# Optimization experiments

Hardware: AMD Instinct MI355X
Metric: run time of the kernel (lower is better)

The kernel has to match this reference:

```python
import jax, jax.numpy as jnp
import numpy as np

B, N, E, D = 1, 50000, 800000, 128


def _mlp(x, w1, b1, w2, b2, w3, b3):
    # MLP(in, hidden, out, l=2): Linear+ReLU, Linear+ReLU, Linear
    h = jax.nn.relu(x @ w1 + b1)
    h = jax.nn.relu(h @ w2 + b2)
    return h @ w3 + b3


def _glorot(key, shape):
    fan_in, fan_out = shape[0], shape[1]
    lim = np.sqrt(6.0 / (fan_in + fan_out)).astype(np.float32)
    return jax.random.uniform(key, shape, jnp.float32, -lim, lim)


def setup_inputs() -> dict:
    key = jax.random.key(0)
    ks = jax.random.split(key, 16)
    inp = {
        "nodes": jax.random.normal(ks[0], (B, N, D), jnp.float32),
        "senders": jax.random.randint(ks[1], (E,), 0, N, jnp.int32),
        "receivers": jax.random.randint(ks[2], (E,), 0, N, jnp.int32),
        # message MLP params: 2D -> D -> D -> D
        "mw1": _glorot(ks[3], (2 * D, D)), "mb1": jnp.zeros((D,), jnp.float32),
        "mw2": _glorot(ks[4], (D, D)),     "mb2": jnp.zeros((D,), jnp.float32),
        "mw3": _glorot(ks[5], (D, D)),     "mb3": jnp.zeros((D,), jnp.float32),
        # node MLP params: 2D -> D -> D -> D
        "nw1": _glorot(ks[6], (2 * D, D)), "nb1": jnp.zeros((D,), jnp.float32),
        "nw2": _glorot(ks[7], (D, D)),     "nb2": jnp.zeros((D,), jnp.float32),
        "nw3": _glorot(ks[8], (D, D)),     "nb3": jnp.zeros((D,), jnp.float32),
    }
    return inp


def reference(nodes, senders, receivers,
              mw1, mb1, mw2, mb2, mw3, mb3,
              nw1, nb1, nw2, nb2, nw3, nb3):
    # gather endpoint features: [B, E, 2D]
    edge_in = jnp.concatenate((nodes[:, receivers], nodes[:, senders]), axis=-1)
    messages = _mlp(edge_in, mw1, mb1, mw2, mb2, mw3, mb3)  # [B, E, D]
    # scatter-add messages into receiver inbox: [B, N, D]
    inbox = jnp.zeros_like(nodes).at[:, receivers].add(messages)
    node_in = jnp.concatenate((nodes, inbox), axis=-1)  # [B, N, 2D]
    return nodes + _mlp(node_in, nw1, nb1, nw2, nb2, nw3, nb3)
```

## Files before the change

### kernel.cpp

```cpp
#include <hip/hip_runtime.h>
#include <hip/hip_bf16.h>
#include <stdint.h>

typedef __bf16 bf16;
typedef bf16 bf16x8 __attribute__((ext_vector_type(8)));
typedef float f32x4 __attribute__((ext_vector_type(4)));

#define N_NODES 50000
#define FEAT 128
#define NB_SCAN ((N_NODES + 1023) / 1024)

static constexpr size_t UV_BYTES    = (size_t)N_NODES * 256 * 2;
static constexpr size_t INBOX_BYTES = (size_t)N_NODES * FEAT * 4;

#define WUV_OFF 0
#define WM2_OFF 32768
#define WM3_OFF 49152
#define WN1_OFF 65536
#define WN2_OFF 98304
#define WN3_OFF 114688
#define W_TOTAL 131072
static constexpr size_t W_BYTES = (size_t)W_TOTAL * 2;
#define PREP_BLOCKS ((W_TOTAL + 255) / 256)

__device__ __forceinline__ bf16x8 cvt_f32x8_bf16(const float* __restrict__ p) {
  float4 f0 = *(const float4*)p;
  float4 f1 = *(const float4*)(p + 4);
  bf16x8 t;
  t[0] = (bf16)f0.x; t[1] = (bf16)f0.y; t[2] = (bf16)f0.z; t[3] = (bf16)f0.w;
  t[4] = (bf16)f1.x; t[5] = (bf16)f1.y; t[6] = (bf16)f1.z; t[7] = (bf16)f1.w;
  return t;
}

__global__ void prep_hist_kernel(const float* __restrict__ mw1, const float* __restrict__ mw2,
                                 const float* __restrict__ mw3, const float* __restrict__ nw1,
                                 const float* __restrict__ nw2, const float* __restrict__ nw3,
                                 bf16* __restrict__ w,
                                 const int* __restrict__ receivers, int* __restrict__ cnt, int E) {
  const int b = blockIdx.x;
  if (b < PREP_BLOCKS) {
    int i = b * 256 + threadIdx.x;
    if (i >= W_TOTAL) return;
    float v;
    if (i < WM2_OFF) {
      int c = i >> 7, k = i & 127;
      v = (c < 128) ? mw1[k * 128 + c] : mw1[(128 + k) * 128 + (c - 128)];
    } else if (i < WM3_OFF) {
      int j = i - WM2_OFF; int c = j >> 7, k = j & 127;
      v = mw2[k * 128 + c];
    } else if (i < WN1_OFF) {
      int j = i - WM3_OFF; int c = j >> 7, k = j & 127;
      v = mw3[k * 128 + c];
    } else if (i < WN2_OFF) {
      int j = i - WN1_OFF; int c = j >> 8, k = j & 255;
      v = nw1[k * 128 + c];
    } else if (i < WN3_OFF) {
      int j = i - WN2_OFF; int c = j >> 7, k = j & 127;
      v = nw2[k * 128 + c];
    } else {
      int j = i - WN3_OFF; int c = j >> 7, k = j & 127;
      v = nw3[k * 128 + c];
    }
    w[i] = (bf16)v;
  } else {
    int i = (b - PREP_BLOCKS) * 256 + threadIdx.x;
    if (i < E) atomicAdd(&cnt[receivers[i]], 1);
  }
}

__global__ __launch_bounds__(1024) void scan1_kernel(const int* __restrict__ cnt,
                                                     int* __restrict__ offs,
                                                     int* __restrict__ bsum) {
  __shared__ int s[1024];
  const int tid = threadIdx.x;
  const int g = blockIdx.x * 1024 + tid;
  int x = (g < N_NODES) ? cnt[g] : 0;
  s[tid] = x;
  __syncthreads();
  for (int off = 1; off < 1024; off <<= 1) {
    int v = (tid >= off) ? s[tid - off] : 0;
    __syncthreads();
    s[tid] += v;
    __syncthreads();
  }
  if (g < N_NODES) offs[g] = s[tid] - x;
  if (tid == 1023) bsum[blockIdx.x] = s[tid];
}

__global__ void scan2_kernel(int* __restrict__ bsum) {
  __shared__ int s[64];
  const int tid = threadIdx.x;
  int x = (tid < NB_SCAN) ? bsum[tid] : 0;
  s[tid] = x;
  __syncthreads();
  for (int off = 1; off < 64; off <<= 1) {
    int v = (tid >= off) ? s[tid - off] : 0;
    __syncthreads();
    s[tid] += v;
    __syncthreads();
  }
  if (tid < NB_SCAN) bsum[tid] = s[tid] - x;
}

__global__ void scatter_inbox_kernel(const int* __restrict__ senders,
                                     const int* __restrict__ receivers,
                                     const int* __restrict__ offs, const int* __restrict__ bsum,
                                     int* __restrict__ cur,
                                     int* __restrict__ sSend, int* __restrict__ sRecv,
                                     const int* __restrict__ cnt, const float* __restrict__ mb3,
                                     float* __restrict__ inbox, int E) {
  const int SC = (E + 255) >> 8;
  const int b = blockIdx.x;
  if (b < SC) {
    int i = b * 256 + threadIdx.x;
    if (i < E) {
      int r = receivers[i];
      int slot = offs[r] + bsum[r >> 10] + atomicAdd(&cur[r], 1);
      sSend[slot] = senders[i];
      sRecv[slot] = r;
    }
  } else {
    int i = (b - SC) * 256 + threadIdx.x;
    if (i >= N_NODES * 32) return;
    int n = i >> 5, q = i & 31;
    float c = (float)cnt[n];
    float4 bb = *(const float4*)(mb3 + q * 4);
    float4 o = {c * bb.x, c * bb.y, c * bb.z, c * bb.w};
    *(float4*)(inbox + (size_t)n * FEAT + q * 4) = o;
  }
}

__global__ __launch_bounds__(512) void uv_gemm_kernel(const float* __restrict__ nodes,
                                                      const bf16* __restrict__ wuvt,
                                                      const float* __restrict__ mb1,
                                                      bf16* __restrict__ uv) {
  const int tid = threadIdx.x;
  const int lane = tid & 63, wid = tid >> 6;
  const int wm = wid >> 2, wn = wid & 3;
  const int rBase = blockIdx.x * 128 + wm * 64;
  const int cBase = wn * 64;
  const int l15 = lane & 15, ka = (lane >> 4) * 8, rj = (lane >> 4) * 4;

  f32x4 acc[4][4];
#pragma unroll
  for (int mi = 0; mi < 4; ++mi)
#pragma unroll
    for (int ni = 0; ni < 4; ++ni) acc[mi][ni] = (f32x4){0.f, 0.f, 0.f, 0.f};

#pragma unroll
  for (int kk = 0; kk < 4; ++kk) {
    const int k0 = kk * 32 + ka;
    bf16x8 a[4], b[4];
#pragma unroll
    for (int mi = 0; mi < 4; ++mi) {
      int r = rBase + mi * 16 + l15;
      if (r > N_NODES - 1) r = N_NODES - 1;
      a[mi] = cvt_f32x8_bf16(nodes + (size_t)r * FEAT + k0);
    }
#pragma unroll
    for (int ni = 0; ni < 4; ++ni) {
      int c = cBase + ni * 16 + l15;
      b[ni] = *(const bf16x8*)(wuvt + (size_t)c * 128 + k0);
    }
#pragma unroll
    for (int mi = 0; mi < 4; ++mi)
#pragma unroll
      for (int ni = 0; ni < 4; ++ni)
        acc[mi][ni] = __builtin_amdgcn_mfma_f32_16x16x32_bf16(a[mi], b[ni], acc[mi][ni], 0, 0, 0);
  }
#pragma unroll
  for (int mi = 0; mi < 4; ++mi)
#pragma unroll
    for (int ni = 0; ni < 4; ++ni) {
      int c = cBase + ni * 16 + l15;
      float bias = (c < FEAT) ? mb1[c] : 0.f;
#pragma unroll
      for (int j = 0; j < 4; ++j) {
        int r = rBase + mi * 16 + rj + j;
        if (r < N_NODES) uv[(size_t)r * 256 + c] = (bf16)(acc[mi][ni][j] + bias);
      }
    }
}

__device__ __forceinline__ void seg_reduce(const f32x4 (&acc3)[2][8], int idr,
                                           int lane, int l15, int rj,
                                           float* __restrict__ inbox) {
  int nxt = __shfl(idr, (lane & 31) + 1);
  bool bnd = ((lane & 31) == 31) || (idr != nxt);
  unsigned long long bm = __ballot(bnd);
  uint32_t mask = (uint32_t)(bm & 0xffffffffull);
  int lo = 0;
  while (mask) {
    int hi = __ffs(mask) - 1;
    mask &= mask - 1;
    int recv = __shfl(idr, hi);
    if (recv >= 0) {
      float s[8];
#pragma unroll
      for (int ni = 0; ni < 8; ++ni) {
        float x = 0.f;
#pragma unroll
        for (int mi = 0; mi < 2; ++mi)
#pragma unroll
          for (int j = 0; j < 4; ++j) {
            int row = mi * 16 + rj + j;
            x += (row >= lo && row <= hi) ? acc3[mi][ni][j] : 0.f;
          }
        x += __shfl_xor(x, 16);
        x += __shfl_xor(x, 32);
        s[ni] = x;
      }
      if (lane < 16) {
        float* dst = inbox + (size_t)recv * FEAT + l15;
#pragma unroll
        for (int ni = 0; ni < 8; ++ni) unsafeAtomicAdd(dst + ni * 16, s[ni]);
      }
    }
    lo = hi + 1;
  }
}

__global__ __launch_bounds__(256, 3) void edge_kernel(const bf16* __restrict__ uv,
                                                      const int* __restrict__ sSend,
                                                      const int* __restrict__ sRecv,
                                                      const bf16* __restrict__ wm2t,
                                                      const bf16* __restrict__ wm3t,
                                                      const float* __restrict__ mb2,
                                                      float* __restrict__ inbox, int E) {
  __shared__ bf16 hbuf[4][16 * 128];
  const int tid = threadIdx.x, lane = tid & 63, wid = tid >> 6;
  const int l15 = lane & 15, ka = (lane >> 4) * 8, rj = (lane >> 4) * 4;
  const int l31 = lane & 31;
  bf16* hw = hbuf[wid];

  const int e0 = (blockIdx.x * 4 + wid) * 32;
  if (e0 >= E) return;

  int e = e0 + l31;
  bool val = e < E;
  int ec = val ? e : E - 1;
  int idr = val ? sRecv[ec] : -1;
  int ids = sSend[ec];

  int rid[2], sid[2];
#pragma unroll
  for (int mi = 0; mi < 2; ++mi) {
    int row = mi * 16 + l15;
    int rv = __shfl(idr, row);
    rid[mi] = rv < 0 ? 0 : rv;
    sid[mi] = __shfl(ids, row);
  }
  bf16x8 afr[2][4];
#pragma unroll
  for (int mi = 0; mi < 2; ++mi) {
    const bf16* up = uv + (size_t)rid[mi] * 256;
    const bf16* vp = uv + (size_t)sid[mi] * 256 + 128;
#pragma unroll
    for (int kk = 0; kk < 4; ++kk) {
      bf16x8 u8 = *(const bf16x8*)(up + kk * 32 + ka);
      bf16x8 v8 = *(const bf16x8*)(vp + kk * 32 + ka);
      bf16x8 h;
#pragma unroll
      for (int x = 0; x < 8; ++x) {
        float s = (float)u8[x] + (float)v8[x];
        h[x] = (bf16)(s > 0.f ? s : 0.f);
      }
      afr[mi][kk] = h;
    }
  }

  f32x4 acc[2][8];
#pragma unroll
  for (int mi = 0; mi < 2; ++mi)
#pragma unroll
    for (int ni = 0; ni < 8; ++ni) acc[mi][ni] = (f32x4){0.f, 0.f, 0.f, 0.f};
  __builtin_amdgcn_s_setprio(1);
#pragma unroll
  for (int kk = 0; kk < 4; ++kk) {
    const int k0 = kk * 32 + ka;
    bf16x8 b[8];
#pragma unroll
    for (int ni = 0; ni < 8; ++ni) {
      int c = ni * 16 + l15;
      b[ni] = *(const bf16x8*)(wm2t + (size_t)c * 128 + k0);
    }
#pragma unroll
    for (int mi = 0; mi < 2; ++mi)
#pragma unroll
      for (int ni = 0; ni < 8; ++ni)
        acc[mi][ni] = __builtin_amdgcn_mfma_f32_16x16x32_bf16(afr[mi][kk], b[ni], acc[mi][ni], 0, 0, 0);
  }
  __builtin_amdgcn_s_setprio(0);

  bf16x8 a3[2][4];
#pragma unroll
  for (int mi = 0; mi < 2; ++mi) {
#pragma unroll
    for (int ni = 0; ni < 8; ++ni) {
      int c = ni * 16 + l15;
      float bias = mb2[c];
#pragma unroll
      for (int j = 0; j < 4; ++j) {
        int row = rj + j;
        float v = acc[mi][ni][j] + bias;
        v = v > 0.f ? v : 0.f;
        int byte = row * 256 + ((c * 2) ^ ((row & 7) << 4));
        *(bf16*)((char*)hw + byte) = (bf16)v;
      }
    }
    asm volatile("s_waitcnt lgkmcnt(0)" ::: "memory");
    __builtin_amdgcn_sched_barrier(0);
#pragma unroll
    for (int kk = 0; kk < 4; ++kk) {
      int k0 = kk * 32 + ka;
      int byte = l15 * 256 + ((k0 * 2) ^ ((l15 & 7) << 4));
      a3[mi][kk] = *(const bf16x8*)((const char*)hw + byte);
    }
    asm volatile("s_waitcnt lgkmcnt(0)" ::: "memory");
    __builtin_amdgcn_sched_barrier(0);
  }

  f32x4 acc3[2][8];
#pragma unroll
  for (int mi = 0; mi < 2; ++mi)
#pragma unroll
    for (int ni = 0; ni < 8; ++ni) acc3[mi][ni] = (f32x4){0.f, 0.f, 0.f, 0.f};
  __builtin_amdgcn_s_setprio(1);
#pragma unroll
  for (int kk = 0; kk < 4; ++kk) {
    const int k0 = kk * 32 + ka;
    bf16x8 b[8];
#pragma unroll
    for (int ni = 0; ni < 8; ++ni) {
      int c = ni * 16 + l15;
      b[ni] = *(const bf16x8*)(wm3t + (size_t)c * 128 + k0);
    }
#pragma unroll
    for (int mi = 0; mi < 2; ++mi)
#pragma unroll
      for (int ni = 0; ni < 8; ++ni)
        acc3[mi][ni] = __builtin_amdgcn_mfma_f32_16x16x32_bf16(a3[mi][kk], b[ni], acc3[mi][ni], 0, 0, 0);
  }
  __builtin_amdgcn_s_setprio(0);

  seg_reduce(acc3, idr, lane, l15, rj, inbox);
}

__global__ __launch_bounds__(256) void node_kernel(const float* __restrict__ nodes,
                                                   const float* __restrict__ inbox,
                                                   const bf16* __restrict__ wn1t,
                                                   const bf16* __restrict__ wn2t,
                                                   const bf16* __restrict__ wn3t,
                                                   const float* __restrict__ nb1,
                                                   const float* __restrict__ nb2,
                                                   const float* __restrict__ nb3,
                                                   float* __restrict__ out) {
  __shared__ bf16 h[128 * 128];
  const int tid = threadIdx.x;
  const int lane = tid & 63, wid = tid >> 6;
  const int wm = wid >> 1, wn = wid & 1;
  const int rBase = wm * 64, cBase = wn * 64;
  const int l15 = lane & 15, ka = (lane >> 4) * 8, rj = (lane >> 4) * 4;
  const int nBase = blockIdx.x * 128;

  f32x4 acc[4][4];
#pragma unroll
  for (int mi = 0; mi < 4; ++mi)
#pragma unroll
    for (int ni = 0; ni < 4; ++ni) acc[mi][ni] = (f32x4){0.f, 0.f, 0.f, 0.f};
#pragma unroll
  for (int kk = 0; kk < 8; ++kk) {
    const int k0 = kk * 32 + ka;
    bf16x8 a[4], b[4];
#pragma unroll
    for (int mi = 0; mi < 4; ++mi) {
      int n = nBase + rBase + mi * 16 + l15;
      if (n > N_NODES - 1) n = N_NODES - 1;
      const float* src = (kk < 4) ? (nodes + (size_t)n * FEAT + k0)
                                  : (inbox + (size_t)n * FEAT + (k0 - 128));
      a[mi] = cvt_f32x8_bf16(src);
    }
#pragma unroll
    for (int ni = 0; ni < 4; ++ni) {
      int c = cBase + ni * 16 + l15;
      b[ni] = *(const bf16x8*)(wn1t + (size_t)c * 256 + k0);
    }
#pragma unroll
    for (int mi = 0; mi < 4; ++mi)
#pragma unroll
      for (int ni = 0; ni < 4; ++ni)
        acc[mi][ni] = __builtin_amdgcn_mfma_f32_16x16x32_bf16(a[mi], b[ni], acc[mi][ni], 0, 0, 0);
  }
#pragma unroll
  for (int mi = 0; mi < 4; ++mi)
#pragma unroll
    for (int ni = 0; ni < 4; ++ni) {
      int c = cBase + ni * 16 + l15;
      float bias = nb1[c];
#pragma unroll
      for (int j = 0; j < 4; ++j) {
        int r = rBase + mi * 16 + rj + j;
        float v = acc[mi][ni][j] + bias;
        v = v > 0.f ? v : 0.f;
        int byte = r * 256 + ((c * 2) ^ ((r & 7) << 4));
        *(bf16*)((char*)h + byte) = (bf16)v;
      }
    }
  __syncthreads();

#pragma unroll
  for (int mi = 0; mi < 4; ++mi)
#pragma unroll
    for (int ni = 0; ni < 4; ++ni) acc[mi][ni] = (f32x4){0.f, 0.f, 0.f, 0.f};
#pragma unroll
  for (int kk = 0; kk < 4; ++kk) {
    const int k0 = kk * 32 + ka;
    bf16x8 a[4], b[4];
#pragma unroll
    for (int mi = 0; mi < 4; ++mi) {
      int r = rBase + mi * 16 + l15;
      int byte = r * 256 + ((k0 * 2) ^ ((r & 7) << 4));
      a[mi] = *(const bf16x8*)((const char*)h + byte);
    }
#pragma unroll
    for (int ni = 0; ni < 4; ++ni) {
      int c = cBase + ni * 16 + l15;
      b[ni] = *(const bf16x8*)(wn2t + (size_t)c * 128 + k0);
    }
#pragma unroll
    for (int mi = 0; mi < 4; ++mi)
#pragma unroll
      for (int ni = 0; ni < 4; ++ni)
        acc[mi][ni] = __builtin_amdgcn_mfma_f32_16x16x32_bf16(a[mi], b[ni], acc[mi][ni], 0, 0, 0);
  }
  __syncthreads();
#pragma unroll
  for (int mi = 0; mi < 4; ++mi)
#pragma unroll
    for (int ni = 0; ni < 4; ++ni) {
      int c = cBase + ni * 16 + l15;
      float bias = nb2[c];
#pragma unroll
      for (int j = 0; j < 4; ++j) {
        int r = rBase + mi * 16 + rj + j;
        float v = acc[mi][ni][j] + bias;
        v = v > 0.f ? v : 0.f;
        int byte = r * 256 + ((c * 2) ^ ((r & 7) << 4));
        *(bf16*)((char*)h + byte) = (bf16)v;
      }
    }
  __syncthreads();

#pragma unroll
  for (int mi = 0; mi < 4; ++mi)
#pragma unroll
    for (int ni = 0; ni < 4; ++ni) acc[mi][ni] = (f32x4){0.f, 0.f, 0.f, 0.f};
#pragma unroll
  for (int kk = 0; kk < 4; ++kk) {
    const int k0 = kk * 32 + ka;
    bf16x8 a[4], b[4];
#pragma unroll
    for (int mi = 0; mi < 4; ++mi) {
      int r = rBase + mi * 16 + l15;
      int byte = r * 256 + ((k0 * 2) ^ ((r & 7) << 4));
      a[mi] = *(const bf16x8*)((const char*)h + byte);
    }
#pragma unroll
    for (int ni = 0; ni < 4; ++ni) {
      int c = cBase + ni * 16 + l15;
      b[ni] = *(const bf16x8*)(wn3t + (size_t)c * 128 + k0);
    }
#pragma unroll
    for (int mi = 0; mi < 4; ++mi)
#pragma unroll
      for (int ni = 0; ni < 4; ++ni)
        acc[mi][ni] = __builtin_amdgcn_mfma_f32_16x16x32_bf16(a[mi], b[ni], acc[mi][ni], 0, 0, 0);
  }
#pragma unroll
  for (int mi = 0; mi < 4; ++mi)
#pragma unroll
    for (int ni = 0; ni < 4; ++ni) {
      int c = cBase + ni * 16 + l15;
      float bias = nb3[c];
#pragma unroll
      for (int j = 0; j < 4; ++j) {
        int r = rBase + mi * 16 + rj + j;
        int n = nBase + r;
        if (n < N_NODES)
          out[(size_t)n * FEAT + c] = nodes[(size_t)n * FEAT + c] + acc[mi][ni][j] + bias;
      }
    }
}

extern "C" void kernel_launch(void* const* d_in, const int* in_sizes, int n_in,
                              void* d_out, int out_size, void* d_ws, size_t ws_size,
                              hipStream_t stream) {
  const float* nodes = (const float*)d_in[0];
  const int* senders = (const int*)d_in[1];
  const int* receivers = (const int*)d_in[2];
  const float* mw1 = (const float*)d_in[3];
  const float* mb1 = (const float*)d_in[4];
  const float* mw2 = (const float*)d_in[5];
  const float* mb2 = (const float*)d_in[6];
  const float* mw3 = (const float*)d_in[7];
  const float* mb3 = (const float*)d_in[8];
  const float* nw1 = (const float*)d_in[9];
  const float* nb1 = (const float*)d_in[10];
  const float* nw2 = (const float*)d_in[11];
  const float* nb2 = (const float*)d_in[12];
  const float* nw3 = (const float*)d_in[13];
  const float* nb3 = (const float*)d_in[14];
  float* out = (float*)d_out;
  const int E = in_sizes[1];

  char* ws = (char*)d_ws;
  bf16* uv = (bf16*)ws;
  bf16* w = (bf16*)(ws + UV_BYTES);
  char* p = ws + UV_BYTES + W_BYTES;
  float* inbox = (float*)p; p += INBOX_BYTES;
  int* offs = (int*)p; p += ((size_t)(N_NODES + 1) * 4 + 255) & ~255ull;
  int* cnt = (int*)p;  p += ((size_t)N_NODES * 4 + 255) & ~255ull;
  int* cur = (int*)p;  p += ((size_t)N_NODES * 4 + 255) & ~255ull;
  int* bsum = (int*)p; p += 256;
  int* sSend = (int*)p; p += ((size_t)E * 4 + 255) & ~255ull;
  int* sRecv = (int*)p; p += ((size_t)E * 4 + 255) & ~255ull;

  const int SC = (E + 255) / 256;
  const int IB = (N_NODES * 32 + 255) / 256;

  hipMemsetAsync(cnt, 0, (size_t)N_NODES * 4, stream);
  hipMemsetAsync(cur, 0, (size_t)N_NODES * 4, stream);
  prep_hist_kernel<<<PREP_BLOCKS + SC, 256, 0, stream>>>(mw1, mw2, mw3, nw1, nw2, nw3, w,
                                                         receivers, cnt, E);
  scan1_kernel<<<NB_SCAN, 1024, 0, stream>>>(cnt, offs, bsum);
  scan2_kernel<<<1, 64, 0, stream>>>(bsum);
  scatter_inbox_kernel<<<SC + IB, 256, 0, stream>>>(senders, receivers, offs, bsum, cur,
                                                    sSend, sRecv, cnt, mb3, inbox, E);
  uv_gemm_kernel<<<(N_NODES + 127) / 128, 512, 0, stream>>>(nodes, w + WUV_OFF, mb1, uv);
  edge_kernel<<<(E + 127) / 128, 256, 0, stream>>>(uv, sSend, sRecv, w + WM2_OFF, w + WM3_OFF,
                                                   mb2, inbox, E);
  node_kernel<<<(N_NODES + 127) / 128, 256, 0, stream>>>(nodes, inbox, w + WN1_OFF, w + WN2_OFF,
                                                         w + WN3_OFF, nb1, nb2, nb3, out);
}
```

Before: 415.5 us.

## Fuse UV GEMM into scatter kernel, merge memsets, XCD-swizzle edge blocks

```diff
diff --git a/kernel.cpp b/kernel.cpp
--- a/kernel.cpp
+++ b/kernel.cpp
@@ -8,7 +8,7 @@
 
 #define N_NODES 50000
 #define FEAT 128
-#define NB_SCAN ((N_NODES + 1023) / 1024)
+#define NB_SCAN ((N_NODES + 511) / 512)
 
 static constexpr size_t UV_BYTES    = (size_t)N_NODES * 256 * 2;
 static constexpr size_t INBOX_BYTES = (size_t)N_NODES * FEAT * 4;
@@ -30,6 +30,12 @@
   t[0] = (bf16)f0.x; t[1] = (bf16)f0.y; t[2] = (bf16)f0.z; t[3] = (bf16)f0.w;
   t[4] = (bf16)f1.x; t[5] = (bf16)f1.y; t[6] = (bf16)f1.z; t[7] = (bf16)f1.w;
   return t;
+}
+
+__device__ __forceinline__ int xcd_swizzle(int bid, int nwg) {
+  int q = nwg >> 3, r = nwg & 7;
+  int xcd = bid & 7, idx = bid >> 3;
+  return (xcd < r ? xcd * (q + 1) : r * (q + 1) + (xcd - r) * q) + idx;
 }
 
 __global__ void prep_hist_kernel(const float* __restrict__ mw1, const float* __restrict__ mw2,
@@ -68,32 +74,32 @@
   }
 }
 
-__global__ __launch_bounds__(1024) void scan1_kernel(const int* __restrict__ cnt,
-                                                     int* __restrict__ offs,
-                                                     int* __restrict__ bsum) {
-  __shared__ int s[1024];
+__global__ __launch_bounds__(512) void scan1_kernel(const int* __restrict__ cnt,
+                                                    int* __restrict__ offs,
+                                                    int* __restrict__ bsum) {
+  __shared__ int s[512];
   const int tid = threadIdx.x;
-  const int g = blockIdx.x * 1024 + tid;
+  const int g = blockIdx.x * 512 + tid;
   int x = (g < N_NODES) ? cnt[g] : 0;
   s[tid] = x;
   __syncthreads();
-  for (int off = 1; off < 1024; off <<= 1) {
+  for (int off = 1; off < 512; off <<= 1) {
     int v = (tid >= off) ? s[tid - off] : 0;
     __syncthreads();
     s[tid] += v;
     __syncthreads();
   }
   if (g < N_NODES) offs[g] = s[tid] - x;
-  if (tid == 1023) bsum[blockIdx.x] = s[tid];
+  if (tid == 511) bsum[blockIdx.x] = s[tid];
 }
 
 __global__ void scan2_kernel(int* __restrict__ bsum) {
-  __shared__ int s[64];
+  __shared__ int s[128];
   const int tid = threadIdx.x;
   int x = (tid < NB_SCAN) ? bsum[tid] : 0;
   s[tid] = x;
   __syncthreads();
-  for (int off = 1; off < 64; off <<= 1) {
+  for (int off = 1; off < 128; off <<= 1) {
     int v = (tid >= off) ? s[tid - off] : 0;
     __syncthreads();
     s[tid] += v;
@@ -102,42 +108,43 @@
   if (tid < NB_SCAN) bsum[tid] = s[tid] - x;
 }
 
-__global__ void scatter_inbox_kernel(const int* __restrict__ senders,
-                                     const int* __restrict__ receivers,
-                                     const int* __restrict__ offs, const int* __restrict__ bsum,
-                                     int* __restrict__ cur,
-                                     int* __restrict__ sSend, int* __restrict__ sRecv,
-                                     const int* __restrict__ cnt, const float* __restrict__ mb3,
-                                     float* __restrict__ inbox, int E) {
-  const int SC = (E + 255) >> 8;
+__global__ __launch_bounds__(512) void scatter_inbox_uv_kernel(
+    const int* __restrict__ senders, const int* __restrict__ receivers,
+    const int* __restrict__ offs, const int* __restrict__ bsum, int* __restrict__ cur,
+    int* __restrict__ sSend, int* __restrict__ sRecv,
+    const int* __restrict__ cnt, const float* __restrict__ mb3, float* __restrict__ inbox,
+    const float* __restrict__ nodes, const bf16* __restrict__ wuvt,
+    const float* __restrict__ mb1, bf16* __restrict__ uv, int E) {
+  const int SC = (E + 511) >> 9;
+  const int IB = (N_NODES * 32 + 511) >> 9;
   const int b = blockIdx.x;
+  const int tid = threadIdx.x;
+
   if (b < SC) {
-    int i = b * 256 + threadIdx.x;
+    int i = b * 512 + tid;
     if (i < E) {
       int r = receivers[i];
-      int slot = offs[r] + bsum[r >> 10] + atomicAdd(&cur[r], 1);
+      int slot = offs[r] + bsum[r >> 9] + atomicAdd(&cur[r], 1);
       sSend[slot] = senders[i];
       sRecv[slot] = r;
     }
-  } else {
-    int i = (b - SC) * 256 + threadIdx.x;
+    return;
+  }
+  if (b < SC + IB) {
+    int i = (b - SC) * 512 + tid;
     if (i >= N_NODES * 32) return;
     int n = i >> 5, q = i & 31;
     float c = (float)cnt[n];
     float4 bb = *(const float4*)(mb3 + q * 4);
     float4 o = {c * bb.x, c * bb.y, c * bb.z, c * bb.w};
     *(float4*)(inbox + (size_t)n * FEAT + q * 4) = o;
-  }
-}
-
-__global__ __launch_bounds__(512) void uv_gemm_kernel(const float* __restrict__ nodes,
-                                                      const bf16* __restrict__ wuvt,
-                                                      const float* __restrict__ mb1,
-                                                      bf16* __restrict__ uv) {
-  const int tid = threadIdx.x;
+    return;
+  }
+
+  const int ub = b - SC - IB;
   const int lane = tid & 63, wid = tid >> 6;
   const int wm = wid >> 2, wn = wid & 3;
-  const int rBase = blockIdx.x * 128 + wm * 64;
+  const int rBase = ub * 128 + wm * 64;
   const int cBase = wn * 64;
   const int l15 = lane & 15, ka = (lane >> 4) * 8, rj = (lane >> 4) * 4;
 
@@ -150,7 +157,7 @@
 #pragma unroll
   for (int kk = 0; kk < 4; ++kk) {
     const int k0 = kk * 32 + ka;
-    bf16x8 a[4], b[4];
+    bf16x8 a[4], bb[4];
 #pragma unroll
     for (int mi = 0; mi < 4; ++mi) {
       int r = rBase + mi * 16 + l15;
@@ -160,13 +167,13 @@
 #pragma unroll
     for (int ni = 0; ni < 4; ++ni) {
       int c = cBase + ni * 16 + l15;
-      b[ni] = *(const bf16x8*)(wuvt + (size_t)c * 128 + k0);
+      bb[ni] = *(const bf16x8*)(wuvt + (size_t)c * 128 + k0);
     }
 #pragma unroll
     for (int mi = 0; mi < 4; ++mi)
 #pragma unroll
       for (int ni = 0; ni < 4; ++ni)
-        acc[mi][ni] = __builtin_amdgcn_mfma_f32_16x16x32_bf16(a[mi], b[ni], acc[mi][ni], 0, 0, 0);
+        acc[mi][ni] = __builtin_amdgcn_mfma_f32_16x16x32_bf16(a[mi], bb[ni], acc[mi][ni], 0, 0, 0);
   }
 #pragma unroll
   for (int mi = 0; mi < 4; ++mi)
@@ -233,7 +240,8 @@
   const int l31 = lane & 31;
   bf16* hw = hbuf[wid];
 
-  const int e0 = (blockIdx.x * 4 + wid) * 32;
+  const int swz = xcd_swizzle(blockIdx.x, gridDim.x);
+  const int e0 = (swz * 4 + wid) * 32;
   if (e0 >= E) return;
 
   int e = e0 + l31;
@@ -519,24 +527,27 @@
   char* p = ws + UV_BYTES + W_BYTES;
   float* inbox = (float*)p; p += INBOX_BYTES;
   int* offs = (int*)p; p += ((size_t)(N_NODES + 1) * 4 + 255) & ~255ull;
-  int* cnt = (int*)p;  p += ((size_t)N_NODES * 4 + 255) & ~255ull;
+  int* cnt = (int*)p;
+  size_t cntPad = ((size_t)N_NODES * 4 + 255) & ~255ull;
+  p += cntPad;
   int* cur = (int*)p;  p += ((size_t)N_NODES * 4 + 255) & ~255ull;
-  int* bsum = (int*)p; p += 256;
+  int* bsum = (int*)p; p += 512;
   int* sSend = (int*)p; p += ((size_t)E * 4 + 255) & ~255ull;
   int* sRecv = (int*)p; p += ((size_t)E * 4 + 255) & ~255ull;
 
-  const int SC = (E + 255) / 256;
-  const int IB = (N_NODES * 32 + 255) / 256;
-
-  hipMemsetAsync(cnt, 0, (size_t)N_NODES * 4, stream);
-  hipMemsetAsync(cur, 0, (size_t)N_NODES * 4, stream);
-  prep_hist_kernel<<<PREP_BLOCKS + SC, 256, 0, stream>>>(mw1, mw2, mw3, nw1, nw2, nw3, w,
+  const int SC = (E + 511) / 512;
+  const int IB = (N_NODES * 32 + 511) / 512;
+  const int UVB = (N_NODES + 127) / 128;
+  const int HB = (E + 255) / 256;
+
+  hipMemsetAsync(cnt, 0, cntPad + (size_t)N_NODES * 4, stream);
+  prep_hist_kernel<<<PREP_BLOCKS + HB, 256, 0, stream>>>(mw1, mw2, mw3, nw1, nw2, nw3, w,
                                                          receivers, cnt, E);
-  scan1_kernel<<<NB_SCAN, 1024, 0, stream>>>(cnt, offs, bsum);
-  scan2_kernel<<<1, 64, 0, stream>>>(bsum);
-  scatter_inbox_kernel<<<SC + IB, 256, 0, stream>>>(senders, receivers, offs, bsum, cur,
-                                                    sSend, sRecv, cnt, mb3, inbox, E);
-  uv_gemm_kernel<<<(N_NODES + 127) / 128, 512, 0, stream>>>(nodes, w + WUV_OFF, mb1, uv);
+  scan1_kernel<<<NB_SCAN, 512, 0, stream>>>(cnt, offs, bsum);
+  scan2_kernel<<<1, 128, 0, stream>>>(bsum);
+  scatter_inbox_uv_kernel<<<SC + IB + UVB, 512, 0, stream>>>(
+      senders, receivers, offs, bsum, cur, sSend, sRecv, cnt, mb3, inbox,
+      nodes, w + WUV_OFF, mb1, uv, E);
   edge_kernel<<<(E + 127) / 128, 256, 0, stream>>>(uv, sSend, sRecv, w + WM2_OFF, w + WM3_OFF,
                                                    mb2, inbox, E);
   node_kernel<<<(N_NODES + 127) / 128, 256, 0, stream>>>(nodes, inbox, w + WN1_OFF, w + WN2_OFF,
```

After: 414.3 us. No clear change (-0.3%).
